# Kernel optimization log

Hardware: AMD Instinct MI355X
Metric: run time of the kernel (lower is better)

Reference implementation:

```python
import jax, jax.numpy as jnp
import numpy as np

B, S, D, H, DK, DV = 2, 2048, 1024, 16, 64, 64
EPS = 1e-5
NEG = -1e9

def setup_inputs() -> dict:
    key = jax.random.key(0)
    ks = jax.random.split(key, 8)
    bound_qkv = (6.0 / D) ** 0.5
    bound_fc = (6.0 / (H * DV)) ** 0.5
    x = jax.random.normal(ks[0], (B, S, D), dtype=jnp.float32)
    # self-attention: Q=K=V inputs (typical decoder usage in this repo)
    input_Q = x
    input_K = jax.random.normal(ks[1], (B, S, D), dtype=jnp.float32)
    input_V = jax.random.normal(ks[2], (B, S, D), dtype=jnp.float32)
    # causal (subsequence) mask, True = masked, as produced by attn_mask()
    causal = jnp.triu(jnp.ones((S, S), dtype=bool), k=1)
    attn_mask = jnp.broadcast_to(causal, (B, S, S))
    W_Q = jax.random.uniform(ks[3], (H * DK, D), jnp.float32, -bound_qkv, bound_qkv)
    W_K = jax.random.uniform(ks[4], (H * DK, D), jnp.float32, -bound_qkv, bound_qkv)
    W_V = jax.random.uniform(ks[5], (H * DV, D), jnp.float32, -bound_qkv, bound_qkv)
    W_fc = jax.random.uniform(ks[6], (D, H * DV), jnp.float32, -bound_fc, bound_fc)
    ln_gamma = jnp.ones((D,), jnp.float32)
    ln_beta = jnp.zeros((D,), jnp.float32)
    return {"input_Q": input_Q, "input_K": input_K, "input_V": input_V,
            "attn_mask": attn_mask, "W_Q": W_Q, "W_K": W_K, "W_V": W_V,
            "W_fc": W_fc, "ln_gamma": ln_gamma, "ln_beta": ln_beta}

def reference(input_Q, input_K, input_V, attn_mask, W_Q, W_K, W_V, W_fc, ln_gamma, ln_beta):
    b = input_Q.shape[0]
    # projections (torch Linear: x @ W.T), reshape to [b, h, s, d]
    Q = (input_Q @ W_Q.T).reshape(b, -1, H, DK).transpose(0, 2, 1, 3)
    K = (input_K @ W_K.T).reshape(b, -1, H, DK).transpose(0, 2, 1, 3)
    V = (input_V @ W_V.T).reshape(b, -1, H, DV).transpose(0, 2, 1, 3)
    scores = jnp.einsum('bhqd,bhkd->bhqk', Q, K) / np.sqrt(DK).astype(np.float32)
    scores = jnp.where(attn_mask[:, None, :, :], NEG, scores)
    softmax_attn = jax.nn.softmax(scores, axis=-1)  # [b, h, q, k]
    qkv = jnp.einsum('bhqk,bhkd->bhqd', softmax_attn, V)
    qkv_out = qkv.transpose(0, 2, 1, 3).reshape(b, -1, H * DV)
    output = qkv_out @ W_fc.T + input_Q  # proj + residual
    mu = jnp.mean(output, axis=-1, keepdims=True)
    var = jnp.var(output, axis=-1, keepdims=True)
    normed = (output - mu) * jax.lax.rsqrt(var + EPS) * ln_gamma + ln_beta
    return normed, softmax_attn
```

## Files before the change

kernel.cpp:

```cpp
#include <hip/hip_runtime.h>
#include <hip/hip_bf16.h>
#include <stdint.h>

#define B_   2
#define S_   2048
#define D_   1024
#define H_   16
#define BH_  32
#define M_   4096
#define PROBS_OFF 4194304ll

typedef __attribute__((ext_vector_type(8))) short short8;
typedef __attribute__((ext_vector_type(4))) float f32x4;

__device__ __forceinline__ short f2bf(float x) {
    uint32_t b = __float_as_uint(x);
    uint32_t r = (b + 0x7FFFu + ((b >> 16) & 1u)) >> 16;
    return (short)r;
}
__device__ __forceinline__ float bf2f(short s) {
    return __uint_as_float(((uint32_t)(uint16_t)s) << 16);
}
__device__ __forceinline__ void split2(float x, short& hi, short& lo) {
    hi = f2bf(x);
    float r = x - bf2f(hi);
    lo = f2bf(r);
}

__global__ __launch_bounds__(256) void k_split(const float* __restrict__ src,
                                               short* __restrict__ hi,
                                               short* __restrict__ lo, int n4) {
    int i = blockIdx.x * 256 + threadIdx.x;
    if (i >= n4) return;
    float4 v = reinterpret_cast<const float4*>(src)[i];
    short h0,l0,h1,l1,h2,l2,h3,l3;
    split2(v.x,h0,l0); split2(v.y,h1,l1); split2(v.z,h2,l2); split2(v.w,h3,l3);
    reinterpret_cast<short4*>(hi)[i] = make_short4(h0,h1,h2,h3);
    reinterpret_cast<short4*>(lo)[i] = make_short4(l0,l1,l2,l3);
}

template<int MODE>
__global__ __launch_bounds__(256) void k_gemm(
    const short* __restrict__ Ahi, const short* __restrict__ Alo,
    const short* __restrict__ Bhi, const short* __restrict__ Blo,
    short* __restrict__ Ohi, short* __restrict__ Olo,
    const float* __restrict__ resid, float* __restrict__ Of)
{
    const int tid = threadIdx.x, w = tid >> 6, lane = tid & 63;
    const int lq = lane & 15, g = lane >> 4;
    const int mbase = blockIdx.y * 128 + (w >> 1) * 64;
    const int nbase = blockIdx.x * 128 + (w & 1) * 64;

    f32x4 acc[4][4];
    #pragma unroll
    for (int i = 0; i < 4; ++i)
        #pragma unroll
        for (int j = 0; j < 4; ++j) acc[i][j] = (f32x4){0.f,0.f,0.f,0.f};

    for (int k0 = 0; k0 < 1024; k0 += 32) {
        short8 ah[4], al[4], bh[4], bl[4];
        #pragma unroll
        for (int mg = 0; mg < 4; ++mg) {
            size_t off = (size_t)(mbase + mg*16 + lq) * 1024 + k0 + g*8;
            ah[mg] = *reinterpret_cast<const short8*>(Ahi + off);
            al[mg] = *reinterpret_cast<const short8*>(Alo + off);
        }
        #pragma unroll
        for (int ng = 0; ng < 4; ++ng) {
            size_t off = (size_t)(nbase + ng*16 + lq) * 1024 + k0 + g*8;
            bh[ng] = *reinterpret_cast<const short8*>(Bhi + off);
            bl[ng] = *reinterpret_cast<const short8*>(Blo + off);
        }
        #pragma unroll
        for (int mg = 0; mg < 4; ++mg)
            #pragma unroll
            for (int ng = 0; ng < 4; ++ng) {
                acc[mg][ng] = __builtin_amdgcn_mfma_f32_16x16x32_bf16(ah[mg], bh[ng], acc[mg][ng], 0,0,0);
                acc[mg][ng] = __builtin_amdgcn_mfma_f32_16x16x32_bf16(ah[mg], bl[ng], acc[mg][ng], 0,0,0);
                acc[mg][ng] = __builtin_amdgcn_mfma_f32_16x16x32_bf16(al[mg], bh[ng], acc[mg][ng], 0,0,0);
            }
    }

    if constexpr (MODE == 3) {
        #pragma unroll
        for (int mg = 0; mg < 4; ++mg)
            #pragma unroll
            for (int ng = 0; ng < 4; ++ng) {
                int n = nbase + ng*16 + lq;
                #pragma unroll
                for (int r = 0; r < 4; ++r) {
                    int m = mbase + mg*16 + g*4 + r;
                    size_t ix = (size_t)m * 1024 + n;
                    Of[ix] = acc[mg][ng][r] + resid[ix];
                }
            }
    } else if constexpr (MODE == 2) {
        #pragma unroll
        for (int mg = 0; mg < 4; ++mg)
            #pragma unroll
            for (int ng = 0; ng < 4; ++ng) {
                int n = nbase + ng*16 + lq;
                int hh = n >> 6, dv = n & 63;
                int m0 = mbase + mg*16 + g*4;
                int bb = m0 >> 11, ss = m0 & 2047;
                size_t idx = (((size_t)bb*16 + hh)*64 + dv) * 2048 + ss;
                uint64_t ph = 0, pl = 0;
                #pragma unroll
                for (int r = 0; r < 4; ++r) {
                    short hbv, lbv; split2(acc[mg][ng][r], hbv, lbv);
                    ph |= (uint64_t)(uint16_t)hbv << (16*r);
                    pl |= (uint64_t)(uint16_t)lbv << (16*r);
                }
                *reinterpret_cast<uint64_t*>(Ohi + idx) = ph;
                *reinterpret_cast<uint64_t*>(Olo + idx) = pl;
            }
    } else {
        #pragma unroll
        for (int mg = 0; mg < 4; ++mg)
            #pragma unroll
            for (int ng = 0; ng < 4; ++ng) {
                int n = nbase + ng*16 + lq;
                int hh = n >> 6, dk = n & 63;
                #pragma unroll
                for (int r = 0; r < 4; ++r) {
                    int m = mbase + mg*16 + g*4 + r;
                    int bb = m >> 11, ss = m & 2047;
                    size_t idx = (((size_t)bb*16 + hh)*2048 + ss) * 64 + dk;
                    short hbv, lbv; split2(acc[mg][ng][r], hbv, lbv);
                    Ohi[idx] = hbv; Olo[idx] = lbv;
                }
            }
    }
}

__global__ __launch_bounds__(256) void k_attn(
    const short* __restrict__ Qhi, const short* __restrict__ Qlo,
    const short* __restrict__ Khi, const short* __restrict__ Klo,
    const short* __restrict__ Vhi, const short* __restrict__ Vlo,
    short* __restrict__ qkvhi, short* __restrict__ qkvlo,
    float* __restrict__ probs)
{
    __shared__ __align__(16) short Ph[4][16][80];
    __shared__ __align__(16) short Pl[4][16][80];

    int flat = blockIdx.x;
    int swz  = (flat & 7) * 128 + (flat >> 3);
    int bh = swz >> 5;
    int qt = swz & 31;

    const int tid = threadIdx.x, w = tid >> 6, lane = tid & 63;
    const int lq = lane & 15, g = lane >> 4;
    const int qbase = qt*64 + w*16;
    const int qrow  = qbase + lq;
    const size_t kvbase = (size_t)bh * S_ * 64;

    short8 qbh[2], qbl[2];
    {
        size_t off = kvbase + (size_t)qrow * 64 + g*8;
        qbh[0] = *reinterpret_cast<const short8*>(Qhi + off);
        qbh[1] = *reinterpret_cast<const short8*>(Qhi + off + 32);
        qbl[0] = *reinterpret_cast<const short8*>(Qlo + off);
        qbl[1] = *reinterpret_cast<const short8*>(Qlo + off + 32);
    }

    auto scores = [&](int kt, float* sv) {
        short8 kfh[4][2], kfl[4][2];
        #pragma unroll
        for (int f = 0; f < 4; ++f)
            #pragma unroll
            for (int c = 0; c < 2; ++c) {
                size_t off = kvbase + (size_t)(kt*64 + f*16 + lq) * 64 + c*32 + g*8;
                kfh[f][c] = *reinterpret_cast<const short8*>(Khi + off);
                kfl[f][c] = *reinterpret_cast<const short8*>(Klo + off);
            }
        f32x4 sa[4];
        #pragma unroll
        for (int f = 0; f < 4; ++f) sa[f] = (f32x4){0.f,0.f,0.f,0.f};
        #pragma unroll
        for (int f = 0; f < 4; ++f)
            #pragma unroll
            for (int c = 0; c < 2; ++c) {
                sa[f] = __builtin_amdgcn_mfma_f32_16x16x32_bf16(kfh[f][c], qbh[c], sa[f], 0,0,0);
                sa[f] = __builtin_amdgcn_mfma_f32_16x16x32_bf16(kfh[f][c], qbl[c], sa[f], 0,0,0);
                sa[f] = __builtin_amdgcn_mfma_f32_16x16x32_bf16(kfl[f][c], qbh[c], sa[f], 0,0,0);
            }
        #pragma unroll
        for (int f = 0; f < 4; ++f)
            #pragma unroll
            for (int r = 0; r < 4; ++r) {
                int k = kt*64 + f*16 + g*4 + r;
                float s = sa[f][r] * 0.125f;
                sv[f*4 + r] = (k <= qrow) ? s : -3e38f;
            }
    };

    float mrun = -3e38f, lrun = 0.f;
    for (int kt = 0; kt <= qt; ++kt) {
        float sv[16];
        scores(kt, sv);
        float tmax = sv[0];
        #pragma unroll
        for (int i = 1; i < 16; ++i) tmax = fmaxf(tmax, sv[i]);
        if (tmax > mrun) { lrun *= __expf(mrun - tmax); mrun = tmax; }
        float ls = 0.f;
        #pragma unroll
        for (int i = 0; i < 16; ++i)
            if (sv[i] > -1e37f) ls += __expf(sv[i] - mrun);
        lrun += ls;
    }
    #pragma unroll
    for (int mk = 16; mk <= 32; mk <<= 1) {
        float mo = __shfl_xor(mrun, mk);
        float lo2 = __shfl_xor(lrun, mk);
        float mn = fmaxf(mrun, mo);
        float e1 = (mrun > -1e37f) ? __expf(mrun - mn) : 0.f;
        float e2 = (mo   > -1e37f) ? __expf(mo   - mn) : 0.f;
        lrun = lrun * e1 + lo2 * e2;
        mrun = mn;
    }
    const float rli = 1.f / lrun;

    f32x4 oacc[4];
    #pragma unroll
    for (int fd = 0; fd < 4; ++fd) oacc[fd] = (f32x4){0.f,0.f,0.f,0.f};
    const size_t pbase = ((size_t)bh * S_ + qrow) * S_;

    for (int kt = 0; kt <= qt; ++kt) {
        float sv[16];
        scores(kt, sv);
        #pragma unroll
        for (int f = 0; f < 4; ++f) {
            float p0 = (sv[f*4+0] > -1e37f) ? __expf(sv[f*4+0] - mrun) * rli : 0.f;
            float p1 = (sv[f*4+1] > -1e37f) ? __expf(sv[f*4+1] - mrun) * rli : 0.f;
            float p2 = (sv[f*4+2] > -1e37f) ? __expf(sv[f*4+2] - mrun) * rli : 0.f;
            float p3 = (sv[f*4+3] > -1e37f) ? __expf(sv[f*4+3] - mrun) * rli : 0.f;
            *reinterpret_cast<float4*>(probs + pbase + kt*64 + f*16 + g*4) =
                make_float4(p0, p1, p2, p3);
            short h0,l0,h1,l1,h2,l2,h3,l3;
            split2(p0,h0,l0); split2(p1,h1,l1); split2(p2,h2,l2); split2(p3,h3,l3);
            uint64_t ph = (uint64_t)(uint16_t)h0 | ((uint64_t)(uint16_t)h1<<16)
                        | ((uint64_t)(uint16_t)h2<<32) | ((uint64_t)(uint16_t)h3<<48);
            uint64_t plw = (uint64_t)(uint16_t)l0 | ((uint64_t)(uint16_t)l1<<16)
                        | ((uint64_t)(uint16_t)l2<<32) | ((uint64_t)(uint16_t)l3<<48);
            *reinterpret_cast<uint64_t*>(&Ph[w][lq][f*16 + g*4]) = ph;
            *reinterpret_cast<uint64_t*>(&Pl[w][lq][f*16 + g*4]) = plw;
        }
        __syncthreads();
        #pragma unroll
        for (int c = 0; c < 2; ++c) {
            short8 pah = *reinterpret_cast<const short8*>(&Ph[w][lq][c*32 + g*8]);
            short8 pal = *reinterpret_cast<const short8*>(&Pl[w][lq][c*32 + g*8]);
            #pragma unroll
            for (int fd = 0; fd < 4; ++fd) {
                size_t voff = kvbase + (size_t)(fd*16 + lq) * 2048 + kt*64 + c*32 + g*8;
                short8 vbh = *reinterpret_cast<const short8*>(Vhi + voff);
                short8 vbl = *reinterpret_cast<const short8*>(Vlo + voff);
                oacc[fd] = __builtin_amdgcn_mfma_f32_16x16x32_bf16(pah, vbh, oacc[fd], 0,0,0);
                oacc[fd] = __builtin_amdgcn_mfma_f32_16x16x32_bf16(pah, vbl, oacc[fd], 0,0,0);
                oacc[fd] = __builtin_amdgcn_mfma_f32_16x16x32_bf16(pal, vbh, oacc[fd], 0,0,0);
            }
        }
        __syncthreads();
    }

    {
        int hh = bh & 15, bb = bh >> 4;
        #pragma unroll
        for (int fd = 0; fd < 4; ++fd)
            #pragma unroll
            for (int r = 0; r < 4; ++r) {
                int n = hh*64 + fd*16 + lq;
                int m = bb*2048 + qbase + g*4 + r;
                size_t ix = (size_t)m * 1024 + n;
                short hbv, lbv; split2(oacc[fd][r], hbv, lbv);
                qkvhi[ix] = hbv; qkvlo[ix] = lbv;
            }
    }

    int kstart = (qt + 1) * 64;
    if (kstart < S_) {
        size_t rowbase = (size_t)bh * S_ * S_ + (size_t)(qt*64) * S_;
        int n4 = (S_ - kstart) >> 2;
        float4 z = make_float4(0.f, 0.f, 0.f, 0.f);
        for (int r = 0; r < 64; ++r) {
            float* rp = probs + rowbase + (size_t)r * S_ + kstart;
            for (int c = tid; c < n4; c += 256)
                reinterpret_cast<float4*>(rp)[c] = z;
        }
    }
}

__global__ __launch_bounds__(256) void k_ln(float* __restrict__ io,
                                            const float* __restrict__ gamma,
                                            const float* __restrict__ beta) {
    int row = blockIdx.x, tid = threadIdx.x;
    size_t base = (size_t)row * 1024 + tid*4;
    float4 v = *reinterpret_cast<const float4*>(io + base);
    float s  = v.x + v.y + v.z + v.w;
    float s2 = v.x*v.x + v.y*v.y + v.z*v.z + v.w*v.w;
    #pragma unroll
    for (int mk = 1; mk < 64; mk <<= 1) { s += __shfl_xor(s, mk); s2 += __shfl_xor(s2, mk); }
    __shared__ float ps[4], ps2[4];
    if ((tid & 63) == 0) { ps[tid>>6] = s; ps2[tid>>6] = s2; }
    __syncthreads();
    s  = ps[0] + ps[1] + ps[2] + ps[3];
    s2 = ps2[0] + ps2[1] + ps2[2] + ps2[3];
    float mean = s * (1.f/1024.f);
    float var  = s2 * (1.f/1024.f) - mean*mean;
    float rstd = rsqrtf(var + 1e-5f);
    float4 gm = *reinterpret_cast<const float4*>(gamma + tid*4);
    float4 bt = *reinterpret_cast<const float4*>(beta  + tid*4);
    float4 o;
    o.x = (v.x - mean)*rstd*gm.x + bt.x;
    o.y = (v.y - mean)*rstd*gm.y + bt.y;
    o.z = (v.z - mean)*rstd*gm.z + bt.z;
    o.w = (v.w - mean)*rstd*gm.w + bt.w;
    *reinterpret_cast<float4*>(io + base) = o;
}

extern "C" void kernel_launch(void* const* d_in, const int* in_sizes, int n_in,
                              void* d_out, int out_size, void* d_ws, size_t ws_size,
                              hipStream_t stream) {
    (void)in_sizes; (void)n_in; (void)out_size; (void)ws_size;
    const float* inQ  = (const float*)d_in[0];
    const float* inK  = (const float*)d_in[1];
    const float* inV  = (const float*)d_in[2];
    const float* WQ   = (const float*)d_in[4];
    const float* WK   = (const float*)d_in[5];
    const float* WV   = (const float*)d_in[6];
    const float* Wfc  = (const float*)d_in[7];
    const float* gam  = (const float*)d_in[8];
    const float* bet  = (const float*)d_in[9];

    float* out    = (float*)d_out;
    float* normed = out;
    float* probs  = out + PROBS_OFF;

    short* p = (short*)d_ws;
    short* Qhi = p;   p += 4194304;  short* Qlo = p;   p += 4194304;
    short* KhiW= p;   p += 4194304;  short* KloW= p;   p += 4194304;
    short* VhiW= p;   p += 4194304;  short* VloW= p;   p += 4194304;
    short* qvh = p;   p += 4194304;  short* qvl = p;   p += 4194304;
    short* Wfh = p;   p += 1048576;  short* Wfl = p;   p += 1048576;

    short* sc = (short*)probs;
    short* Xqh = sc;  sc += 4194304;  short* Xql = sc;  sc += 4194304;
    short* Xkh = sc;  sc += 4194304;  short* Xkl = sc;  sc += 4194304;
    short* Xvh = sc;  sc += 4194304;  short* Xvl = sc;  sc += 4194304;
    short* Wqh = sc;  sc += 1048576;  short* Wql = sc;  sc += 1048576;
    short* Wkh = sc;  sc += 1048576;  short* Wkl = sc;  sc += 1048576;
    short* Wvh = sc;  sc += 1048576;  short* Wvl = sc;  sc += 1048576;

    k_split<<<4096, 256, 0, stream>>>(inQ, Xqh, Xql, 1048576);
    k_split<<<4096, 256, 0, stream>>>(inK, Xkh, Xkl, 1048576);
    k_split<<<4096, 256, 0, stream>>>(inV, Xvh, Xvl, 1048576);
    k_split<<<1024, 256, 0, stream>>>(WQ,  Wqh, Wql, 262144);
    k_split<<<1024, 256, 0, stream>>>(WK,  Wkh, Wkl, 262144);
    k_split<<<1024, 256, 0, stream>>>(WV,  Wvh, Wvl, 262144);
    k_split<<<1024, 256, 0, stream>>>(Wfc, Wfh, Wfl, 262144);

    dim3 gg(8, 32);
    k_gemm<0><<<gg, 256, 0, stream>>>(Xqh, Xql, Wqh, Wql, Qhi,  Qlo,  nullptr, nullptr);
    k_gemm<0><<<gg, 256, 0, stream>>>(Xkh, Xkl, Wkh, Wkl, KhiW, KloW, nullptr, nullptr);
    k_gemm<2><<<gg, 256, 0, stream>>>(Xvh, Xvl, Wvh, Wvl, VhiW, VloW, nullptr, nullptr);

    k_attn<<<1024, 256, 0, stream>>>(Qhi, Qlo, KhiW, KloW, VhiW, VloW, qvh, qvl, probs);

    k_gemm<3><<<gg, 256, 0, stream>>>(qvh, qvl, Wfh, Wfl, nullptr, nullptr, inQ, normed);

    k_ln<<<4096, 256, 0, stream>>>(normed, gam, bet);
}
```

Before: 1.376 ms.

## Stage GEMM tiles through double-buffered LDS via global_load_lds and merge split launches

The projection and output GEMMs now copy 128x32 hi/lo tiles of A and B into double-buffered shared memory with async global-to-LDS loads, prefetching the next k-slice while the current one feeds the MFMAs. Previously every wave read its fragments straight from global memory, so tiles shared across waves were fetched repeatedly. The seven split launches are also merged into two kernels to cut launch overhead. LDS fragment reads use a 64-byte row stride, which may cause bank conflicts, and the single barrier per iteration must order the buffer reuse correctly.

Result: faster. 1.293 ms (-6.1%).

```diff
diff --git a/kernel.cpp b/kernel.cpp
--- a/kernel.cpp
+++ b/kernel.cpp
@@ -27,16 +27,43 @@
     lo = f2bf(r);
 }
 
-__global__ __launch_bounds__(256) void k_split(const float* __restrict__ src,
-                                               short* __restrict__ hi,
-                                               short* __restrict__ lo, int n4) {
-    int i = blockIdx.x * 256 + threadIdx.x;
-    if (i >= n4) return;
-    float4 v = reinterpret_cast<const float4*>(src)[i];
+typedef const __attribute__((address_space(1))) char ga_char;
+typedef __attribute__((address_space(3))) char la_char;
+__device__ __forceinline__ void gld_lds16(const void* g, void* l) {
+    __builtin_amdgcn_global_load_lds((ga_char*)g, (la_char*)l, 16, 0, 0);
+}
+
+__device__ __forceinline__ void split_store(const float* s, short* h, short* l, int j) {
+    float4 v = reinterpret_cast<const float4*>(s)[j];
     short h0,l0,h1,l1,h2,l2,h3,l3;
     split2(v.x,h0,l0); split2(v.y,h1,l1); split2(v.z,h2,l2); split2(v.w,h3,l3);
-    reinterpret_cast<short4*>(hi)[i] = make_short4(h0,h1,h2,h3);
-    reinterpret_cast<short4*>(lo)[i] = make_short4(l0,l1,l2,l3);
+    reinterpret_cast<short4*>(h)[j] = make_short4(h0,h1,h2,h3);
+    reinterpret_cast<short4*>(l)[j] = make_short4(l0,l1,l2,l3);
+}
+__global__ __launch_bounds__(256) void k_split3(
+    const float* __restrict__ s0, const float* __restrict__ s1, const float* __restrict__ s2,
+    short* __restrict__ h0, short* __restrict__ l0, short* __restrict__ h1,
+    short* __restrict__ l1, short* __restrict__ h2, short* __restrict__ l2)
+{
+    int i = blockIdx.x * 256 + threadIdx.x;
+    int which = i >> 20, j = i & ((1 << 20) - 1);
+    const float* s = which == 0 ? s0 : which == 1 ? s1 : s2;
+    short* h = which == 0 ? h0 : which == 1 ? h1 : h2;
+    short* l = which == 0 ? l0 : which == 1 ? l1 : l2;
+    split_store(s, h, l, j);
+}
+__global__ __launch_bounds__(256) void k_split4(
+    const float* __restrict__ s0, const float* __restrict__ s1,
+    const float* __restrict__ s2, const float* __restrict__ s3,
+    short* __restrict__ h0, short* __restrict__ l0, short* __restrict__ h1, short* __restrict__ l1,
+    short* __restrict__ h2, short* __restrict__ l2, short* __restrict__ h3, short* __restrict__ l3)
+{
+    int i = blockIdx.x * 256 + threadIdx.x;
+    int which = i >> 18, j = i & ((1 << 18) - 1);
+    const float* s = which == 0 ? s0 : which == 1 ? s1 : which == 2 ? s2 : s3;
+    short* h = which == 0 ? h0 : which == 1 ? h1 : which == 2 ? h2 : h3;
+    short* l = which == 0 ? l0 : which == 1 ? l1 : which == 2 ? l2 : l3;
+    split_store(s, h, l, j);
 }
 
 template<int MODE>
@@ -46,10 +73,28 @@
     short* __restrict__ Ohi, short* __restrict__ Olo,
     const float* __restrict__ resid, float* __restrict__ Of)
 {
+    __shared__ __align__(16) short sA[2][2][4096];
+    __shared__ __align__(16) short sB[2][2][4096];
+
     const int tid = threadIdx.x, w = tid >> 6, lane = tid & 63;
     const int lq = lane & 15, g = lane >> 4;
-    const int mbase = blockIdx.y * 128 + (w >> 1) * 64;
-    const int nbase = blockIdx.x * 128 + (w & 1) * 64;
+    const int mtile = blockIdx.y * 128, ntile = blockIdx.x * 128;
+    const int mbase = (w >> 1) * 64, nbase = (w & 1) * 64;
+
+    const char* Ah = (const char*)Ahi + (size_t)mtile * 2048;
+    const char* Al = (const char*)Alo + (size_t)mtile * 2048;
+    const char* Bh = (const char*)Bhi + (size_t)ntile * 2048;
+    const char* Bl = (const char*)Blo + (size_t)ntile * 2048;
+
+    auto stage = [&](const char* srcbase, short* dst) {
+        char* d = (char*)dst;
+        #pragma unroll
+        for (int i = 0; i < 2; ++i) {
+            uint32_t o = (uint32_t)((i*256 + tid) * 16);
+            uint32_t row = o >> 6, col = o & 63u;
+            gld_lds16(srcbase + (size_t)row * 2048 + col, d + o);
+        }
+    };
 
     f32x4 acc[4][4];
     #pragma unroll
@@ -57,19 +102,29 @@
         #pragma unroll
         for (int j = 0; j < 4; ++j) acc[i][j] = (f32x4){0.f,0.f,0.f,0.f};
 
-    for (int k0 = 0; k0 < 1024; k0 += 32) {
+    stage(Ah, sA[0][0]); stage(Al, sA[0][1]);
+    stage(Bh, sB[0][0]); stage(Bl, sB[0][1]);
+
+    for (int ki = 0; ki < 32; ++ki) {
+        __syncthreads();
+        int cur = ki & 1;
+        if (ki < 31) {
+            size_t kb = (size_t)(ki + 1) * 64;
+            stage(Ah + kb, sA[cur^1][0]); stage(Al + kb, sA[cur^1][1]);
+            stage(Bh + kb, sB[cur^1][0]); stage(Bl + kb, sB[cur^1][1]);
+        }
         short8 ah[4], al[4], bh[4], bl[4];
         #pragma unroll
         for (int mg = 0; mg < 4; ++mg) {
-            size_t off = (size_t)(mbase + mg*16 + lq) * 1024 + k0 + g*8;
-            ah[mg] = *reinterpret_cast<const short8*>(Ahi + off);
-            al[mg] = *reinterpret_cast<const short8*>(Alo + off);
+            size_t a = (size_t)(mbase + mg*16 + lq) * 64 + g*16;
+            ah[mg] = *reinterpret_cast<const short8*>((const char*)sA[cur][0] + a);
+            al[mg] = *reinterpret_cast<const short8*>((const char*)sA[cur][1] + a);
         }
         #pragma unroll
         for (int ng = 0; ng < 4; ++ng) {
-            size_t off = (size_t)(nbase + ng*16 + lq) * 1024 + k0 + g*8;
-            bh[ng] = *reinterpret_cast<const short8*>(Bhi + off);
-            bl[ng] = *reinterpret_cast<const short8*>(Blo + off);
+            size_t a = (size_t)(nbase + ng*16 + lq) * 64 + g*16;
+            bh[ng] = *reinterpret_cast<const short8*>((const char*)sB[cur][0] + a);
+            bl[ng] = *reinterpret_cast<const short8*>((const char*)sB[cur][1] + a);
         }
         #pragma unroll
         for (int mg = 0; mg < 4; ++mg)
@@ -81,15 +136,16 @@
             }
     }
 
+    const int gm0 = mtile + mbase, gn0 = ntile + nbase;
     if constexpr (MODE == 3) {
         #pragma unroll
         for (int mg = 0; mg < 4; ++mg)
             #pragma unroll
             for (int ng = 0; ng < 4; ++ng) {
-                int n = nbase + ng*16 + lq;
+                int n = gn0 + ng*16 + lq;
                 #pragma unroll
                 for (int r = 0; r < 4; ++r) {
-                    int m = mbase + mg*16 + g*4 + r;
+                    int m = gm0 + mg*16 + g*4 + r;
                     size_t ix = (size_t)m * 1024 + n;
                     Of[ix] = acc[mg][ng][r] + resid[ix];
                 }
@@ -99,9 +155,9 @@
         for (int mg = 0; mg < 4; ++mg)
             #pragma unroll
             for (int ng = 0; ng < 4; ++ng) {
-                int n = nbase + ng*16 + lq;
+                int n = gn0 + ng*16 + lq;
                 int hh = n >> 6, dv = n & 63;
-                int m0 = mbase + mg*16 + g*4;
+                int m0 = gm0 + mg*16 + g*4;
                 int bb = m0 >> 11, ss = m0 & 2047;
                 size_t idx = (((size_t)bb*16 + hh)*64 + dv) * 2048 + ss;
                 uint64_t ph = 0, pl = 0;
@@ -119,11 +175,11 @@
         for (int mg = 0; mg < 4; ++mg)
             #pragma unroll
             for (int ng = 0; ng < 4; ++ng) {
-                int n = nbase + ng*16 + lq;
+                int n = gn0 + ng*16 + lq;
                 int hh = n >> 6, dk = n & 63;
                 #pragma unroll
                 for (int r = 0; r < 4; ++r) {
-                    int m = mbase + mg*16 + g*4 + r;
+                    int m = gm0 + mg*16 + g*4 + r;
                     int bb = m >> 11, ss = m & 2047;
                     size_t idx = (((size_t)bb*16 + hh)*2048 + ss) * 64 + dk;
                     short hbv, lbv; split2(acc[mg][ng][r], hbv, lbv);
@@ -351,13 +407,8 @@
     short* Wkh = sc;  sc += 1048576;  short* Wkl = sc;  sc += 1048576;
     short* Wvh = sc;  sc += 1048576;  short* Wvl = sc;  sc += 1048576;
 
-    k_split<<<4096, 256, 0, stream>>>(inQ, Xqh, Xql, 1048576);
-    k_split<<<4096, 256, 0, stream>>>(inK, Xkh, Xkl, 1048576);
-    k_split<<<4096, 256, 0, stream>>>(inV, Xvh, Xvl, 1048576);
-    k_split<<<1024, 256, 0, stream>>>(WQ,  Wqh, Wql, 262144);
-    k_split<<<1024, 256, 0, stream>>>(WK,  Wkh, Wkl, 262144);
-    k_split<<<1024, 256, 0, stream>>>(WV,  Wvh, Wvl, 262144);
-    k_split<<<1024, 256, 0, stream>>>(Wfc, Wfh, Wfl, 262144);
+    k_split3<<<12288, 256, 0, stream>>>(inQ, inK, inV, Xqh, Xql, Xkh, Xkl, Xvh, Xvl);
+    k_split4<<<4096, 256, 0, stream>>>(WQ, WK, WV, Wfc, Wqh, Wql, Wkh, Wkl, Wvh, Wvl, Wfh, Wfl);
 
     dim3 gg(8, 32);
     k_gemm<0><<<gg, 256, 0, stream>>>(Xqh, Xql, Wqh, Wql, Qhi,  Qlo,  nullptr, nullptr);
```
